# Performance work log

Measured on AMD Instinct MI355X. Metric: run time of the kernel, lower is better.

## Reference

```python
import jax, jax.numpy as jnp
import numpy as np

B, F, C_IN, C_OUT, W_DIM, K2, PAD = 4, 98304, 256, 3, 512, 4, 4096
N = B * F  # total real faces across batch


def setup_inputs() -> dict:
    key = jax.random.key(0)
    ks = jax.random.split(key, 5)
    x = jax.random.normal(ks[0], (N, C_IN), jnp.float32)
    face_neighborhood = jax.random.randint(ks[1], (N, K2), 0, N + PAD)
    # pads placed at the end of the padded slot array (exactly PAD true entries)
    face_is_pad = jnp.concatenate([jnp.zeros((N,), bool), jnp.ones((PAD,), bool)])
    w = jax.random.normal(ks[2], (B, W_DIM), jnp.float32)
    affine_weight = jax.random.normal(ks[3], (C_IN, W_DIM), jnp.float32)
    affine_bias = jnp.ones((C_IN,), jnp.float32)  # bias_init=1
    weight = jax.random.normal(ks[4], (C_OUT, C_IN, 1, K2), jnp.float32)
    bias = jnp.zeros((C_OUT,), jnp.float32)
    return dict(x=x, face_neighborhood=face_neighborhood, face_is_pad=face_is_pad,
                pad_size=PAD, w=w, affine_weight=affine_weight,
                affine_bias=affine_bias, weight=weight, bias=bias)


def reference(x, face_neighborhood, face_is_pad, pad_size, w,
              affine_weight, affine_bias, weight, bias):
    weight_gain = 1.0 / np.sqrt(C_IN * K2)
    # FullyConnectedLayer (stylegan2-ada): out = w @ (A.T / sqrt(in)) + bias(=1)
    styles = (w @ (affine_weight.T / np.float32(np.sqrt(W_DIM))) + affine_bias) * weight_gain  # [B, C_in]
    # create_faceconv_input: scatter real features into padded slots (pads = 0)
    real_rank = jnp.cumsum(~face_is_pad) - 1                      # [N+pad] rank among real slots
    padded = jnp.where(face_is_pad[:, None], jnp.float32(0),
                       x[jnp.clip(real_rank, 0, N - 1)])           # [N+pad, C_in]
    gathered = padded[face_neighborhood]                           # [N, K2, C_in]
    g = gathered.reshape(B, F, K2, C_IN)
    # modulated_face_conv, demodulate=False:
    # out[b,f,o] = sum_{c,k} g[b,f,k,c] * weight[o,c,0,k] * styles[b,c]
    out = jnp.einsum('bfkc,ock,bc->bfo', g, weight[:, :, 0, :], styles)
    out = out.reshape(N, C_OUT) + bias[None, :]
    return jnp.clip(out, -256.0, 256.0)
```

## Files before the change

kernel.cpp:

```cpp
#include <hip/hip_runtime.h>
#include <hip/hip_bf16.h>


#define N_FACES   393216
#define C_IN      256
#define C_OUT     3
#define W_DIM     512
#define K2        4
#define BATCH     4
#define F_PER_B   98304
#define NJ        48
#define ZSLOTS    64

typedef __attribute__((ext_vector_type(8))) short bf16x8;
typedef __attribute__((ext_vector_type(4))) float f32x4;

static __device__ __forceinline__ float bfbits2f(unsigned int hi16) {
    union { unsigned int u; float f; } v; v.u = hi16;
    return v.f;
}

__global__ __launch_bounds__(256) void wmod_bf16_kernel(
    const float* __restrict__ w,
    const float* __restrict__ aw,
    const float* __restrict__ ab,
    const float* __restrict__ weight,
    unsigned short* __restrict__ wmodT)
{
    int t = blockIdx.x * blockDim.x + threadIdx.x;
    if (t >= BATCH * C_IN) return;
    int b = t >> 8;
    int c = t & 255;

    const float* wr = w  + b * W_DIM;
    const float* ar = aw + c * W_DIM;
    float acc = 0.f;
    #pragma unroll 4
    for (int d = 0; d < W_DIM; d += 4) {
        float4 wv = *reinterpret_cast<const float4*>(wr + d);
        float4 av = *reinterpret_cast<const float4*>(ar + d);
        acc += wv.x * av.x + wv.y * av.y + wv.z * av.z + wv.w * av.w;
    }
    const float rsqrt_wdim = 0.04419417382415922f;
    const float gain       = 0.03125f;
    float s = (acc * rsqrt_wdim + ab[c]) * gain;

    #pragma unroll
    for (int o = 0; o < C_OUT; ++o)
        #pragma unroll
        for (int k = 0; k < K2; ++k) {
            int j = b * (K2 * C_OUT) + k * C_OUT + o;
            union { __hip_bfloat16 h; unsigned short u; } cv;
            cv.h = __float2bfloat16(weight[(o * C_IN + c) * K2 + k] * s);
            wmodT[j * C_IN + c] = cv.u;
        }
}

#define LDW 264

__global__ __launch_bounds__(256) void gemm_z_kernel(
    const float*          __restrict__ x,
    const unsigned short* __restrict__ wmodT,
    unsigned short*       __restrict__ z)
{
    __shared__ __align__(16) unsigned short bs[NJ][LDW];
    __shared__ __align__(16) unsigned short zs[4][16][ZSLOTS];

    {
        unsigned int* p = reinterpret_cast<unsigned int*>(&zs[0][0][0]);
        #pragma unroll
        for (int i = 0; i < 8; ++i) p[threadIdx.x + 256 * i] = 0u;
    }
    const unsigned int* g = reinterpret_cast<const unsigned int*>(wmodT);
    for (int i = threadIdx.x; i < NJ * (C_IN / 2); i += 256) {
        int r = i >> 7;
        int c = i & 127;
        reinterpret_cast<unsigned int*>(&bs[r][0])[c] = g[r * 128 + c];
    }
    __syncthreads();

    const int wave = threadIdx.x >> 6;
    const int lane = threadIdx.x & 63;
    const int tile = blockIdx.x * 4 + wave;
    const int row  = lane & 15;
    const int kq   = lane >> 4;

    const float* xrow = x + (size_t)(tile * 16 + row) * C_IN + kq * 8;

    f32x4 acc0 = {0.f, 0.f, 0.f, 0.f};
    f32x4 acc1 = {0.f, 0.f, 0.f, 0.f};
    f32x4 acc2 = {0.f, 0.f, 0.f, 0.f};

    #pragma unroll
    for (int ks = 0; ks < 8; ++ks) {
        const float4* p = reinterpret_cast<const float4*>(xrow + ks * 32);
        float4 a0 = p[0];
        float4 a1 = p[1];
        union { bf16x8 v; __hip_bfloat16 h[8]; } af;
        af.h[0] = __float2bfloat16(a0.x); af.h[1] = __float2bfloat16(a0.y);
        af.h[2] = __float2bfloat16(a0.z); af.h[3] = __float2bfloat16(a0.w);
        af.h[4] = __float2bfloat16(a1.x); af.h[5] = __float2bfloat16(a1.y);
        af.h[6] = __float2bfloat16(a1.z); af.h[7] = __float2bfloat16(a1.w);

        const int cofs = ks * 32 + kq * 8;
        bf16x8 b0 = *reinterpret_cast<const bf16x8*>(&bs[ 0 + row][cofs]);
        bf16x8 b1 = *reinterpret_cast<const bf16x8*>(&bs[16 + row][cofs]);
        bf16x8 b2 = *reinterpret_cast<const bf16x8*>(&bs[32 + row][cofs]);

        acc0 = __builtin_amdgcn_mfma_f32_16x16x32_bf16(af.v, b0, acc0, 0, 0, 0);
        acc1 = __builtin_amdgcn_mfma_f32_16x16x32_bf16(af.v, b1, acc1, 0, 0, 0);
        acc2 = __builtin_amdgcn_mfma_f32_16x16x32_bf16(af.v, b2, acc2, 0, 0, 0);
    }

    const int colj = lane & 15;
    int slot[3];
    #pragma unroll
    for (int a = 0; a < 3; ++a) {
        int j   = a * 16 + colj;
        int b   = j / 12;
        int rem = j - b * 12;
        slot[a] = b * 16 + rem + rem / 3;
    }
    #pragma unroll
    for (int r = 0; r < 4; ++r) {
        const int lr = kq * 4 + r;
        union { __hip_bfloat16 h; unsigned short u; } c0, c1, c2;
        c0.h = __float2bfloat16(acc0[r]);
        c1.h = __float2bfloat16(acc1[r]);
        c2.h = __float2bfloat16(acc2[r]);
        zs[wave][lr][slot[0]] = c0.u;
        zs[wave][lr][slot[1]] = c1.u;
        zs[wave][lr][slot[2]] = c2.u;
    }
    __syncthreads();

    const int rrow = lane >> 2;
    const int rchk = lane & 3;
    const uint4* lp = reinterpret_cast<const uint4*>(&zs[wave][rrow][rchk * 16]);
    uint4 v0 = lp[0];
    uint4 v1 = lp[1];
    uint4* zp = reinterpret_cast<uint4*>(z + (size_t)(tile * 16 + rrow) * ZSLOTS + rchk * 16);
    zp[0] = v0;
    zp[1] = v1;
}

__global__ __launch_bounds__(256) void gather_out_kernel(
    const int*            __restrict__ nb,
    const unsigned short* __restrict__ z,
    const float*          __restrict__ bias,
    float*                __restrict__ out)
{
    int n = blockIdx.x * 256 + threadIdx.x;
    if (n >= N_FACES) return;
    int b = n / F_PER_B;

    const int4 idx4 = *reinterpret_cast<const int4*>(nb + n * K2);
    int ids[K2] = { idx4.x, idx4.y, idx4.z, idx4.w };

    float s0 = 0.f, s1 = 0.f, s2 = 0.f;
    #pragma unroll
    for (int k = 0; k < K2; ++k) {
        int id = ids[k];
        if (id < N_FACES) {
            uint2 v = *reinterpret_cast<const uint2*>(
                z + (size_t)id * ZSLOTS + b * 16 + k * 4);
            s0 += bfbits2f(v.x << 16);
            s1 += bfbits2f(v.x & 0xffff0000u);
            s2 += bfbits2f(v.y << 16);
        }
    }
    s0 = fminf(fmaxf(s0 + bias[0], -256.f), 256.f);
    s1 = fminf(fmaxf(s1 + bias[1], -256.f), 256.f);
    s2 = fminf(fmaxf(s2 + bias[2], -256.f), 256.f);
    float* po = out + (size_t)n * C_OUT;
    po[0] = s0; po[1] = s1; po[2] = s2;
}

__global__ __launch_bounds__(256) void wmod_kernel(
    const float* __restrict__ w, const float* __restrict__ aw,
    const float* __restrict__ ab, const float* __restrict__ weight,
    float* __restrict__ wmod)
{
    int t = blockIdx.x * blockDim.x + threadIdx.x;
    if (t >= BATCH * C_IN) return;
    int b = t >> 8, c = t & 255;
    const float* wr = w + b * W_DIM;
    const float* ar = aw + c * W_DIM;
    float acc = 0.f;
    #pragma unroll 4
    for (int d = 0; d < W_DIM; d += 4) {
        float4 wv = *reinterpret_cast<const float4*>(wr + d);
        float4 av = *reinterpret_cast<const float4*>(ar + d);
        acc += wv.x * av.x + wv.y * av.y + wv.z * av.z + wv.w * av.w;
    }
    float s = (acc * 0.04419417382415922f + ab[c]) * 0.03125f;
    #pragma unroll
    for (int o = 0; o < C_OUT; ++o)
        #pragma unroll
        for (int k = 0; k < K2; ++k)
            wmod[(((b * K2 + k) * C_OUT + o) << 8) + c] =
                weight[(o * C_IN + c) * K2 + k] * s;
}

__global__ __launch_bounds__(256) void face_conv_kernel(
    const float* __restrict__ x, const int* __restrict__ nb,
    const float* __restrict__ wmod, const float* __restrict__ bias,
    float* __restrict__ out)
{
    const int n    = (blockIdx.x * blockDim.x + threadIdx.x) >> 6;
    const int lane = threadIdx.x & 63;
    if (n >= N_FACES) return;
    const int b = n / F_PER_B;
    const int4 idx4 = *reinterpret_cast<const int4*>(nb + n * K2);
    int idx[K2] = { idx4.x, idx4.y, idx4.z, idx4.w };
    const int cofs = lane << 2;
    const float* wm = wmod + ((b * K2 * C_OUT) << 8) + cofs;
    float acc0 = 0.f, acc1 = 0.f, acc2 = 0.f;
    #pragma unroll
    for (int k = 0; k < K2; ++k) {
        const int id = idx[k];
        if (id < N_FACES) {
            const float4 xv = *reinterpret_cast<const float4*>(x + (size_t)id * C_IN + cofs);
            const float* wk = wm + ((k * C_OUT) << 8);
            const float4 w0 = *reinterpret_cast<const float4*>(wk);
            const float4 w1 = *reinterpret_cast<const float4*>(wk + 256);
            const float4 w2 = *reinterpret_cast<const float4*>(wk + 512);
            acc0 += xv.x * w0.x + xv.y * w0.y + xv.z * w0.z + xv.w * w0.w;
            acc1 += xv.x * w1.x + xv.y * w1.y + xv.z * w1.z + xv.w * w1.w;
            acc2 += xv.x * w2.x + xv.y * w2.y + xv.z * w2.z + xv.w * w2.w;
        }
    }
    #pragma unroll
    for (int off = 32; off > 0; off >>= 1) {
        acc0 += __shfl_xor(acc0, off, 64);
        acc1 += __shfl_xor(acc1, off, 64);
        acc2 += __shfl_xor(acc2, off, 64);
    }
    if (lane < C_OUT) {
        float v = (lane == 0) ? acc0 : (lane == 1) ? acc1 : acc2;
        v += bias[lane];
        v = fminf(fmaxf(v, -256.f), 256.f);
        out[n * C_OUT + lane] = v;
    }
}

extern "C" void kernel_launch(void* const* d_in, const int* in_sizes, int n_in,
                              void* d_out, int out_size, void* d_ws, size_t ws_size,
                              hipStream_t stream)
{
    const float* x      = (const float*)d_in[0];
    const int*   nb     = (const int*)  d_in[1];
    const float* w      = (const float*)d_in[4];
    const float* aw     = (const float*)d_in[5];
    const float* ab     = (const float*)d_in[6];
    const float* weight = (const float*)d_in[7];
    const float* bias   = (const float*)d_in[8];
    float*       out    = (float*)d_out;

    const size_t zoff   = 32768;
    const size_t zbytes = (size_t)N_FACES * ZSLOTS * sizeof(unsigned short);

    if (ws_size >= zoff + zbytes) {
        unsigned short* wmodT = (unsigned short*)d_ws;
        unsigned short* z     = (unsigned short*)((char*)d_ws + zoff);

        wmod_bf16_kernel<<<(BATCH * C_IN + 255) / 256, 256, 0, stream>>>(
            w, aw, ab, weight, wmodT);

        gemm_z_kernel<<<(N_FACES / 16) / 4, 256, 0, stream>>>(x, wmodT, z);

        gather_out_kernel<<<N_FACES / 256, 256, 0, stream>>>(nb, z, bias, out);
    } else {
        float* wmod = (float*)d_ws;
        wmod_kernel<<<(BATCH * C_IN + 255) / 256, 256, 0, stream>>>(
            w, aw, ab, weight, wmod);
        face_conv_kernel<<<N_FACES / 4, 256, 0, stream>>>(x, nb, wmod, bias, out);
    }
}
```

Before: 144.1 us.

## Persistent GEMM grid with zero-padded z rows, drop LDS staging and pad branch

```diff
diff --git a/kernel.cpp b/kernel.cpp
--- a/kernel.cpp
+++ b/kernel.cpp
@@ -2,15 +2,19 @@
 #include <hip/hip_bf16.h>
 
 
-#define N_FACES   393216
-#define C_IN      256
-#define C_OUT     3
-#define W_DIM     512
-#define K2        4
-#define BATCH     4
-#define F_PER_B   98304
-#define NJ        48
-#define ZSLOTS    64
+#define N_FACES    393216
+#define C_IN       256
+#define C_OUT      3
+#define W_DIM      512
+#define K2         4
+#define BATCH      4
+#define F_PER_B    98304
+#define NJ         48
+#define ZSLOTS     64
+#define PAD        4096
+#define REAL_TILES 24576
+#define TOT_TILES  24832
+#define GEMM_BLOCKS 1536
 
 typedef __attribute__((ext_vector_type(8))) short bf16x8;
 typedef __attribute__((ext_vector_type(4))) float f32x4;
@@ -64,13 +68,7 @@
     unsigned short*       __restrict__ z)
 {
     __shared__ __align__(16) unsigned short bs[NJ][LDW];
-    __shared__ __align__(16) unsigned short zs[4][16][ZSLOTS];
-
-    {
-        unsigned int* p = reinterpret_cast<unsigned int*>(&zs[0][0][0]);
-        #pragma unroll
-        for (int i = 0; i < 8; ++i) p[threadIdx.x + 256 * i] = 0u;
-    }
+
     const unsigned int* g = reinterpret_cast<const unsigned int*>(wmodT);
     for (int i = threadIdx.x; i < NJ * (C_IN / 2); i += 256) {
         int r = i >> 7;
@@ -81,38 +79,10 @@
 
     const int wave = threadIdx.x >> 6;
     const int lane = threadIdx.x & 63;
-    const int tile = blockIdx.x * 4 + wave;
     const int row  = lane & 15;
     const int kq   = lane >> 4;
-
-    const float* xrow = x + (size_t)(tile * 16 + row) * C_IN + kq * 8;
-
-    f32x4 acc0 = {0.f, 0.f, 0.f, 0.f};
-    f32x4 acc1 = {0.f, 0.f, 0.f, 0.f};
-    f32x4 acc2 = {0.f, 0.f, 0.f, 0.f};
-
-    #pragma unroll
-    for (int ks = 0; ks < 8; ++ks) {
-        const float4* p = reinterpret_cast<const float4*>(xrow + ks * 32);
-        float4 a0 = p[0];
-        float4 a1 = p[1];
-        union { bf16x8 v; __hip_bfloat16 h[8]; } af;
-        af.h[0] = __float2bfloat16(a0.x); af.h[1] = __float2bfloat16(a0.y);
-        af.h[2] = __float2bfloat16(a0.z); af.h[3] = __float2bfloat16(a0.w);
-        af.h[4] = __float2bfloat16(a1.x); af.h[5] = __float2bfloat16(a1.y);
-        af.h[6] = __float2bfloat16(a1.z); af.h[7] = __float2bfloat16(a1.w);
-
-        const int cofs = ks * 32 + kq * 8;
-        bf16x8 b0 = *reinterpret_cast<const bf16x8*>(&bs[ 0 + row][cofs]);
-        bf16x8 b1 = *reinterpret_cast<const bf16x8*>(&bs[16 + row][cofs]);
-        bf16x8 b2 = *reinterpret_cast<const bf16x8*>(&bs[32 + row][cofs]);
-
-        acc0 = __builtin_amdgcn_mfma_f32_16x16x32_bf16(af.v, b0, acc0, 0, 0, 0);
-        acc1 = __builtin_amdgcn_mfma_f32_16x16x32_bf16(af.v, b1, acc1, 0, 0, 0);
-        acc2 = __builtin_amdgcn_mfma_f32_16x16x32_bf16(af.v, b2, acc2, 0, 0, 0);
-    }
-
     const int colj = lane & 15;
+
     int slot[3];
     #pragma unroll
     for (int a = 0; a < 3; ++a) {
@@ -121,27 +91,55 @@
         int rem = j - b * 12;
         slot[a] = b * 16 + rem + rem / 3;
     }
-    #pragma unroll
-    for (int r = 0; r < 4; ++r) {
-        const int lr = kq * 4 + r;
-        union { __hip_bfloat16 h; unsigned short u; } c0, c1, c2;
-        c0.h = __float2bfloat16(acc0[r]);
-        c1.h = __float2bfloat16(acc1[r]);
-        c2.h = __float2bfloat16(acc2[r]);
-        zs[wave][lr][slot[0]] = c0.u;
-        zs[wave][lr][slot[1]] = c1.u;
-        zs[wave][lr][slot[2]] = c2.u;
-    }
-    __syncthreads();
-
-    const int rrow = lane >> 2;
-    const int rchk = lane & 3;
-    const uint4* lp = reinterpret_cast<const uint4*>(&zs[wave][rrow][rchk * 16]);
-    uint4 v0 = lp[0];
-    uint4 v1 = lp[1];
-    uint4* zp = reinterpret_cast<uint4*>(z + (size_t)(tile * 16 + rrow) * ZSLOTS + rchk * 16);
-    zp[0] = v0;
-    zp[1] = v1;
+
+    for (int gt = blockIdx.x * 4 + wave; gt < TOT_TILES; gt += GEMM_BLOCKS * 4) {
+        if (gt < REAL_TILES) {
+            const float* xrow = x + (size_t)(gt * 16 + row) * C_IN + kq * 8;
+
+            f32x4 acc0 = {0.f, 0.f, 0.f, 0.f};
+            f32x4 acc1 = {0.f, 0.f, 0.f, 0.f};
+            f32x4 acc2 = {0.f, 0.f, 0.f, 0.f};
+
+            #pragma unroll
+            for (int ks = 0; ks < 8; ++ks) {
+                const float4* p = reinterpret_cast<const float4*>(xrow + ks * 32);
+                float4 a0 = p[0];
+                float4 a1 = p[1];
+                union { bf16x8 v; __hip_bfloat16 h[8]; } af;
+                af.h[0] = __float2bfloat16(a0.x); af.h[1] = __float2bfloat16(a0.y);
+                af.h[2] = __float2bfloat16(a0.z); af.h[3] = __float2bfloat16(a0.w);
+                af.h[4] = __float2bfloat16(a1.x); af.h[5] = __float2bfloat16(a1.y);
+                af.h[6] = __float2bfloat16(a1.z); af.h[7] = __float2bfloat16(a1.w);
+
+                const int cofs = ks * 32 + kq * 8;
+                bf16x8 b0 = *reinterpret_cast<const bf16x8*>(&bs[ 0 + row][cofs]);
+                bf16x8 b1 = *reinterpret_cast<const bf16x8*>(&bs[16 + row][cofs]);
+                bf16x8 b2 = *reinterpret_cast<const bf16x8*>(&bs[32 + row][cofs]);
+
+                acc0 = __builtin_amdgcn_mfma_f32_16x16x32_bf16(af.v, b0, acc0, 0, 0, 0);
+                acc1 = __builtin_amdgcn_mfma_f32_16x16x32_bf16(af.v, b1, acc1, 0, 0, 0);
+                acc2 = __builtin_amdgcn_mfma_f32_16x16x32_bf16(af.v, b2, acc2, 0, 0, 0);
+            }
+
+            #pragma unroll
+            for (int r = 0; r < 4; ++r) {
+                size_t zr = (size_t)(gt * 16 + kq * 4 + r) * ZSLOTS;
+                union { __hip_bfloat16 h; unsigned short u; } c0, c1, c2;
+                c0.h = __float2bfloat16(acc0[r]);
+                c1.h = __float2bfloat16(acc1[r]);
+                c2.h = __float2bfloat16(acc2[r]);
+                z[zr + slot[0]] = c0.u;
+                z[zr + slot[1]] = c1.u;
+                z[zr + slot[2]] = c2.u;
+            }
+        } else {
+            unsigned short* zp = z + (size_t)(gt * 16 + (lane >> 2)) * ZSLOTS
+                                   + (lane & 3) * 16;
+            uint4 zero = {0u, 0u, 0u, 0u};
+            *reinterpret_cast<uint4*>(zp)     = zero;
+            *reinterpret_cast<uint4*>(zp + 8) = zero;
+        }
+    }
 }
 
 __global__ __launch_bounds__(256) void gather_out_kernel(
@@ -160,14 +158,11 @@
     float s0 = 0.f, s1 = 0.f, s2 = 0.f;
     #pragma unroll
     for (int k = 0; k < K2; ++k) {
-        int id = ids[k];
-        if (id < N_FACES) {
-            uint2 v = *reinterpret_cast<const uint2*>(
-                z + (size_t)id * ZSLOTS + b * 16 + k * 4);
-            s0 += bfbits2f(v.x << 16);
-            s1 += bfbits2f(v.x & 0xffff0000u);
-            s2 += bfbits2f(v.y << 16);
-        }
+        uint2 v = *reinterpret_cast<const uint2*>(
+            z + (size_t)ids[k] * ZSLOTS + b * 16 + k * 4);
+        s0 += bfbits2f(v.x << 16);
+        s1 += bfbits2f(v.x & 0xffff0000u);
+        s2 += bfbits2f(v.y << 16);
     }
     s0 = fminf(fmaxf(s0 + bias[0], -256.f), 256.f);
     s1 = fminf(fmaxf(s1 + bias[1], -256.f), 256.f);
@@ -258,7 +253,7 @@
     float*       out    = (float*)d_out;
 
     const size_t zoff   = 32768;
-    const size_t zbytes = (size_t)N_FACES * ZSLOTS * sizeof(unsigned short);
+    const size_t zbytes = (size_t)TOT_TILES * 16 * ZSLOTS * sizeof(unsigned short);
 
     if (ws_size >= zoff + zbytes) {
         unsigned short* wmodT = (unsigned short*)d_ws;
@@ -267,7 +262,7 @@
         wmod_bf16_kernel<<<(BATCH * C_IN + 255) / 256, 256, 0, stream>>>(
             w, aw, ab, weight, wmodT);
 
-        gemm_z_kernel<<<(N_FACES / 16) / 4, 256, 0, stream>>>(x, wmodT, z);
+        gemm_z_kernel<<<GEMM_BLOCKS, 256, 0, stream>>>(x, wmodT, z);
 
         gather_out_kernel<<<N_FACES / 256, 256, 0, stream>>>(nb, z, bias, out);
     } else {
```

After: 145.4 us. Within noise of the previous version (+0.9%).
